# Performance work log

Hardware: AMD Instinct MI355X
Metric: run time of the kernel (lower is better)

The kernel has to match this reference:

```python
import jax, jax.numpy as jnp
import numpy as np

N_NODES = 50000
N_EDGES = 800000
D_IN, H1, H2, D_OUT = 96, 32, 64, 128
BN_EPS = 1e-5
LRELU_SLOPE = 0.01


def setup_inputs() -> dict:
    key = jax.random.key(0)
    ks = jax.random.split(key, 6)
    x = jax.random.normal(ks[0], (N_NODES, D_IN), dtype=jnp.float32)
    edge_index = jax.random.randint(ks[1], (2, N_EDGES), 0, N_NODES, dtype=jnp.int64)
    # MLP params (Linear: y = x @ W + b), Kaiming-ish scale
    W1 = jax.random.normal(ks[2], (D_IN, H1), dtype=jnp.float32) * (1.0 / np.sqrt(D_IN))
    b1 = jnp.zeros((H1,), dtype=jnp.float32)
    W2 = jax.random.normal(ks[3], (H1, H2), dtype=jnp.float32) * (1.0 / np.sqrt(H1))
    b2 = jnp.zeros((H2,), dtype=jnp.float32)
    W3 = jax.random.normal(ks[4], (H2, D_OUT), dtype=jnp.float32) * (1.0 / np.sqrt(H2))
    b3 = jnp.zeros((D_OUT,), dtype=jnp.float32)
    gamma = jnp.ones((D_OUT,), dtype=jnp.float32)
    beta = jnp.zeros((D_OUT,), dtype=jnp.float32)
    return {"x": x, "edge_index": edge_index, "W1": W1, "b1": b1,
            "W2": W2, "b2": b2, "W3": W3, "b3": b3,
            "gamma": gamma, "beta": beta}


def reference(x, edge_index, W1, b1, W2, b2, W3, b3, gamma, beta):
    src, dst = edge_index[0], edge_index[1]
    # GIN aggregation (eps=0, sum): h_i = x_i + sum_{j -> i} x_j
    agg = jax.ops.segment_sum(x[src], dst, num_segments=x.shape[0])  # [N, D_IN]
    h = x + agg
    # MLP: Linear-Sigmoid-Linear-Sigmoid-Linear
    h = jax.nn.sigmoid(h @ W1 + b1)
    h = jax.nn.sigmoid(h @ W2 + b2)
    h = h @ W3 + b3
    # final activation: LeakyReLU(negative_slope=0.01)
    h = jnp.where(h >= 0, h, LRELU_SLOPE * h)
    # BatchNorm1d over nodes (training mode, biased variance)
    mean = jnp.mean(h, axis=0)
    var = jnp.mean(jnp.square(h - mean), axis=0)
    h = (h - mean) * jax.lax.rsqrt(var + BN_EPS) * gamma + beta
    return (h, edge_index)
```

## Files before the change

kernel.cpp:

```cpp
#include <hip/hip_runtime.h>
#include <hip/hip_bf16.h>

#define N_NODES 50000
#define N_EDGES 800000
#define D_IN 96
#define H1 32
#define H2 64
#define D_OUT 128
#define BN_EPS 1e-5f
#define SLOPE 0.01f
#define MAXDEG 64

__device__ __forceinline__ float sigmoidf(float v) {
    return 1.0f / (1.0f + __expf(-v));
}

__global__ void zero_kernel(int* __restrict__ p, int n) {
    int i = blockIdx.x * blockDim.x + threadIdx.x;
    if (i < n) p[i] = 0;
}

__global__ __launch_bounds__(256) void scatter_kernel(const int* __restrict__ ei,
                                                      int* __restrict__ deg,
                                                      int* __restrict__ csr) {
    int e = blockIdx.x * 256 + threadIdx.x;
    if (e >= N_EDGES) return;
    int src = ei[e];
    int dst = ei[N_EDGES + e];
    int pos = atomicAdd(&deg[dst], 1);
    if (pos < MAXDEG) csr[dst * MAXDEG + pos] = src;
}

__global__ __launch_bounds__(256) void gather_mlp_kernel(
    const float* __restrict__ x, const int* __restrict__ deg,
    const int* __restrict__ csr,
    const float* __restrict__ W1, const float* __restrict__ b1,
    const float* __restrict__ W2, const float* __restrict__ b2,
    const float* __restrict__ W3, const float* __restrict__ b3,
    float* __restrict__ out) {
    __shared__ float hl[8 * D_IN];
    __shared__ float a1l[8 * H1];
    __shared__ float a2l[8 * H2];

    int tid = threadIdx.x;
    int s = tid >> 5;
    int f = tid & 31;
    int node = blockIdx.x * 8 + s;

    const float* xn = x + (size_t)node * D_IN;
    float h0 = xn[f];
    float h1 = xn[32 + f];
    float h2 = xn[64 + f];
    int cnt = deg[node];
    if (cnt > MAXDEG) cnt = MAXDEG;
    const int* lst = csr + (size_t)node * MAXDEG;
    for (int e = 0; e < cnt; ++e) {
        int src = lst[e];
        const float* xr = x + (size_t)src * D_IN;
        h0 += xr[f];
        h1 += xr[32 + f];
        h2 += xr[64 + f];
    }
    float* hs = hl + s * D_IN;
    hs[f] = h0; hs[32 + f] = h1; hs[64 + f] = h2;
    __syncthreads();

    float acc = b1[f];
#pragma unroll 8
    for (int k = 0; k < D_IN; ++k)
        acc = fmaf(hs[k], W1[k * H1 + f], acc);
    a1l[s * H1 + f] = sigmoidf(acc);
    __syncthreads();

    const float* a1s = a1l + s * H1;
    float2 acc2 = reinterpret_cast<const float2*>(b2)[f];
#pragma unroll 8
    for (int k = 0; k < H1; ++k) {
        float a = a1s[k];
        float2 w = reinterpret_cast<const float2*>(W2 + k * H2)[f];
        acc2.x = fmaf(a, w.x, acc2.x);
        acc2.y = fmaf(a, w.y, acc2.y);
    }
    a2l[s * H2 + 2 * f]     = sigmoidf(acc2.x);
    a2l[s * H2 + 2 * f + 1] = sigmoidf(acc2.y);
    __syncthreads();

    const float* a2s = a2l + s * H2;
    float4 acc4 = reinterpret_cast<const float4*>(b3)[f];
#pragma unroll 8
    for (int k = 0; k < H2; ++k) {
        float a = a2s[k];
        float4 w = reinterpret_cast<const float4*>(W3 + k * D_OUT)[f];
        acc4.x = fmaf(a, w.x, acc4.x);
        acc4.y = fmaf(a, w.y, acc4.y);
        acc4.z = fmaf(a, w.z, acc4.z);
        acc4.w = fmaf(a, w.w, acc4.w);
    }
    float4 v;
    v.x = acc4.x >= 0.0f ? acc4.x : SLOPE * acc4.x;
    v.y = acc4.y >= 0.0f ? acc4.y : SLOPE * acc4.y;
    v.z = acc4.z >= 0.0f ? acc4.z : SLOPE * acc4.z;
    v.w = acc4.w >= 0.0f ? acc4.w : SLOPE * acc4.w;
    reinterpret_cast<float4*>(out + (size_t)node * D_OUT)[f] = v;
}

#define RPB 250
__global__ __launch_bounds__(256) void reduce_kernel(const float* __restrict__ out,
                                                     float* __restrict__ sums) {
    __shared__ float ps[256], ps2[256];
    int tid = threadIdx.x;
    int f = tid & 127;
    int g = tid >> 7;
    int base = blockIdx.x * RPB;
    float s = 0.0f, s2 = 0.0f;
    for (int r = g; r < RPB; r += 2) {
        float v = out[(size_t)(base + r) * D_OUT + f];
        s += v;
        s2 += v * v;
    }
    ps[tid] = s; ps2[tid] = s2;
    __syncthreads();
    if (tid < 128) {
        s = ps[tid] + ps[tid + 128];
        s2 = ps2[tid] + ps2[tid + 128];
        atomicAdd(&sums[f], s);
        atomicAdd(&sums[D_OUT + f], s2);
    }
}

__global__ __launch_bounds__(256) void bn_copy_kernel(float* __restrict__ out,
                                                      const float* __restrict__ sums,
                                                      const float* __restrict__ gamma,
                                                      const float* __restrict__ beta,
                                                      const int* __restrict__ ei) {
    int i = blockIdx.x * 256 + threadIdx.x;
    const int NOUT0 = N_NODES * D_OUT;
    const int NTOT = NOUT0 + 2 * N_EDGES;
    if (i >= NTOT) return;
    if (i < NOUT0) {
        int f = i & (D_OUT - 1);
        const float invN = 1.0f / (float)N_NODES;
        float m = sums[f] * invN;
        float var = sums[D_OUT + f] * invN - m * m;
        float inv = rsqrtf(var + BN_EPS);
        out[i] = (out[i] - m) * inv * gamma[f] + beta[f];
    } else {
        out[i] = (float)ei[i - NOUT0];
    }
}

extern "C" void kernel_launch(void* const* d_in, const int* in_sizes, int n_in,
                              void* d_out, int out_size, void* d_ws, size_t ws_size,
                              hipStream_t stream) {
    const float* x = (const float*)d_in[0];
    const int* ei = (const int*)d_in[1];
    const float* W1 = (const float*)d_in[2];
    const float* b1 = (const float*)d_in[3];
    const float* W2 = (const float*)d_in[4];
    const float* b2 = (const float*)d_in[5];
    const float* W3 = (const float*)d_in[6];
    const float* b3 = (const float*)d_in[7];
    const float* gamma = (const float*)d_in[8];
    const float* beta = (const float*)d_in[9];

    float* out = (float*)d_out;
    float* sums = (float*)d_ws;
    int* deg = (int*)(sums + 2 * D_OUT);
    int* csr = deg + N_NODES;

    const int n_zero = 2 * D_OUT + N_NODES;
    zero_kernel<<<(n_zero + 255) / 256, 256, 0, stream>>>((int*)d_ws, n_zero);

    scatter_kernel<<<(N_EDGES + 255) / 256, 256, 0, stream>>>(ei, deg, csr);

    gather_mlp_kernel<<<N_NODES / 8, 256, 0, stream>>>(
        x, deg, csr, W1, b1, W2, b2, W3, b3, out);

    reduce_kernel<<<N_NODES / RPB, 256, 0, stream>>>(out, sums);

    const int n_total = N_NODES * D_OUT + 2 * N_EDGES;
    bn_copy_kernel<<<(n_total + 255) / 256, 256, 0, stream>>>(out, sums, gamma, beta, ei);
}
```

Baseline: 314.1 us.

## Apply first linear layer before aggregation and gather projected features

```diff
diff --git a/kernel.cpp b/kernel.cpp
--- a/kernel.cpp
+++ b/kernel.cpp
@@ -22,23 +22,41 @@
 
 __global__ __launch_bounds__(256) void scatter_kernel(const int* __restrict__ ei,
                                                       int* __restrict__ deg,
-                                                      int* __restrict__ csr) {
+                                                      unsigned short* __restrict__ csr) {
     int e = blockIdx.x * 256 + threadIdx.x;
     if (e >= N_EDGES) return;
     int src = ei[e];
     int dst = ei[N_EDGES + e];
     int pos = atomicAdd(&deg[dst], 1);
-    if (pos < MAXDEG) csr[dst * MAXDEG + pos] = src;
+    if (pos < MAXDEG) csr[(size_t)dst * MAXDEG + pos] = (unsigned short)src;
+}
+
+__global__ __launch_bounds__(256) void gemm1_kernel(const float* __restrict__ x,
+                                                    const float* __restrict__ W1,
+                                                    float* __restrict__ y) {
+    __shared__ float xs[8 * D_IN];
+    int tid = threadIdx.x;
+    int base = blockIdx.x * 8 * D_IN;
+    xs[tid]       = x[base + tid];
+    xs[tid + 256] = x[base + tid + 256];
+    xs[tid + 512] = x[base + tid + 512];
+    __syncthreads();
+    int s = tid >> 5, f = tid & 31;
+    const float* xr = xs + s * D_IN;
+    float acc = 0.0f;
+#pragma unroll 8
+    for (int k = 0; k < D_IN; ++k)
+        acc = fmaf(xr[k], W1[k * H1 + f], acc);
+    y[(size_t)blockIdx.x * 256 + tid] = acc;
 }
 
 __global__ __launch_bounds__(256) void gather_mlp_kernel(
-    const float* __restrict__ x, const int* __restrict__ deg,
-    const int* __restrict__ csr,
-    const float* __restrict__ W1, const float* __restrict__ b1,
+    const float* __restrict__ y, const int* __restrict__ deg,
+    const unsigned short* __restrict__ csr,
+    const float* __restrict__ b1,
     const float* __restrict__ W2, const float* __restrict__ b2,
     const float* __restrict__ W3, const float* __restrict__ b3,
     float* __restrict__ out) {
-    __shared__ float hl[8 * D_IN];
     __shared__ float a1l[8 * H1];
     __shared__ float a2l[8 * H2];
 
@@ -47,28 +65,22 @@
     int f = tid & 31;
     int node = blockIdx.x * 8 + s;
 
-    const float* xn = x + (size_t)node * D_IN;
-    float h0 = xn[f];
-    float h1 = xn[32 + f];
-    float h2 = xn[64 + f];
+    float acc = y[(size_t)node * H1 + f] + b1[f];
     int cnt = deg[node];
     if (cnt > MAXDEG) cnt = MAXDEG;
-    const int* lst = csr + (size_t)node * MAXDEG;
-    for (int e = 0; e < cnt; ++e) {
-        int src = lst[e];
-        const float* xr = x + (size_t)src * D_IN;
-        h0 += xr[f];
-        h1 += xr[32 + f];
-        h2 += xr[64 + f];
+    const unsigned short* lst = csr + (size_t)node * MAXDEG;
+    int e = 0;
+    for (; e + 4 <= cnt; e += 4) {
+        ushort4 s4 = *reinterpret_cast<const ushort4*>(lst + e);
+        float v0 = y[(size_t)s4.x * H1 + f];
+        float v1 = y[(size_t)s4.y * H1 + f];
+        float v2 = y[(size_t)s4.z * H1 + f];
+        float v3 = y[(size_t)s4.w * H1 + f];
+        acc += (v0 + v1) + (v2 + v3);
     }
-    float* hs = hl + s * D_IN;
-    hs[f] = h0; hs[32 + f] = h1; hs[64 + f] = h2;
-    __syncthreads();
+    for (; e < cnt; ++e)
+        acc += y[(size_t)lst[e] * H1 + f];
 
-    float acc = b1[f];
-#pragma unroll 8
-    for (int k = 0; k < D_IN; ++k)
-        acc = fmaf(hs[k], W1[k * H1 + f], acc);
     a1l[s * H1 + f] = sigmoidf(acc);
     __syncthreads();
 
@@ -166,15 +178,18 @@
     float* out = (float*)d_out;
     float* sums = (float*)d_ws;
     int* deg = (int*)(sums + 2 * D_OUT);
-    int* csr = deg + N_NODES;
+    float* y = (float*)(deg + N_NODES);
+    unsigned short* csr = (unsigned short*)(y + (size_t)N_NODES * H1);
 
     const int n_zero = 2 * D_OUT + N_NODES;
     zero_kernel<<<(n_zero + 255) / 256, 256, 0, stream>>>((int*)d_ws, n_zero);
 
     scatter_kernel<<<(N_EDGES + 255) / 256, 256, 0, stream>>>(ei, deg, csr);
 
+    gemm1_kernel<<<N_NODES / 8, 256, 0, stream>>>(x, W1, y);
+
     gather_mlp_kernel<<<N_NODES / 8, 256, 0, stream>>>(
-        x, deg, csr, W1, b1, W2, b2, W3, b3, out);
+        y, deg, csr, b1, W2, b2, W3, b3, out);
 
     reduce_kernel<<<N_NODES / RPB, 256, 0, stream>>>(out, sums);
 
```

After: 295.0 us. 6.1% less time.
